# Optimization experiments

Measured on AMD Instinct MI355X. Metric: run time of the kernel, lower is better.

The kernel has to match this reference:

```python
import jax, jax.numpy as jnp
import numpy as np

N_NODES = 100000
N_EDGES = 1600000
IN_F = 16
C1, C2 = 32, 64
HID = 128
N_CLASSES = 10
NUM_LAYERS = 3


def setup_inputs() -> dict:
    key = jax.random.key(0)
    ks = jax.random.split(key, 20)
    s = 0.1
    inp = {
        "x": jax.random.normal(ks[0], (N_NODES, IN_F), dtype=jnp.float32),
        "edge_index": jax.random.randint(ks[1], (2, N_EDGES), 0, N_NODES, dtype=jnp.int64),
        "edge_attr": jax.random.uniform(ks[2], (N_EDGES, 1), dtype=jnp.float32),
        # conv1 (out=32): per-step weight [L, 32, 32], GRUCell params
        "W1": jax.random.normal(ks[3], (NUM_LAYERS, C1, C1), dtype=jnp.float32) * s,
        "Wih1": jax.random.normal(ks[4], (3 * C1, C1), dtype=jnp.float32) * s,
        "Whh1": jax.random.normal(ks[5], (3 * C1, C1), dtype=jnp.float32) * s,
        "bih1": jnp.zeros((3 * C1,), dtype=jnp.float32),
        "bhh1": jnp.zeros((3 * C1,), dtype=jnp.float32),
        # conv2 (out=64)
        "W2": jax.random.normal(ks[6], (NUM_LAYERS, C2, C2), dtype=jnp.float32) * s,
        "Wih2": jax.random.normal(ks[7], (3 * C2, C2), dtype=jnp.float32) * s,
        "Whh2": jax.random.normal(ks[8], (3 * C2, C2), dtype=jnp.float32) * s,
        "bih2": jnp.zeros((3 * C2,), dtype=jnp.float32),
        "bhh2": jnp.zeros((3 * C2,), dtype=jnp.float32),
        # MLP head
        "fc1_w": jax.random.normal(ks[9], (HID, C2), dtype=jnp.float32) * s,
        "fc1_b": jnp.zeros((HID,), dtype=jnp.float32),
        "fc2_w": jax.random.normal(ks[10], (N_CLASSES, HID), dtype=jnp.float32) * s,
        "fc2_b": jnp.zeros((N_CLASSES,), dtype=jnp.float32),
    }
    return inp


def _gru_cell(m, h, Wih, Whh, bih, bhh):
    gi = m @ Wih.T + bih
    gh = h @ Whh.T + bhh
    ir, iz, inn = jnp.split(gi, 3, axis=1)
    hr, hz, hn = jnp.split(gh, 3, axis=1)
    r = jax.nn.sigmoid(ir + hr)
    z = jax.nn.sigmoid(iz + hz)
    n = jnp.tanh(inn + r * hn)
    return (1.0 - z) * n + z * h


def _gated_graph_conv(x, edge_index, edge_weight, W, Wih, Whh, bih, bhh):
    # PyG GatedGraphConv with aggr='max'
    n, c = x.shape
    out_ch = W.shape[-1]
    h = jnp.pad(x, ((0, 0), (0, out_ch - c))) if c < out_ch else x
    src, dst = edge_index[0], edge_index[1]
    ew = edge_weight[:, None]
    for i in range(W.shape[0]):
        m = h @ W[i]
        msg = m[src] * ew                      # [E, out_ch] gather + scale
        agg = jax.ops.segment_max(msg, dst, num_segments=n)  # scatter-max
        agg = jnp.where(jnp.isfinite(agg), agg, 0.0)         # empty segs -> 0
        h = _gru_cell(agg, h, Wih, Whh, bih, bhh)
    return h


def reference(x, edge_index, edge_attr, W1, Wih1, Whh1, bih1, bhh1,
              W2, Wih2, Whh2, bih2, bhh2, fc1_w, fc1_b, fc2_w, fc2_b):
    ew = jnp.squeeze(edge_attr)
    h = jax.nn.elu(_gated_graph_conv(x, edge_index, ew, W1, Wih1, Whh1, bih1, bhh1))
    h = jax.nn.elu(_gated_graph_conv(h, edge_index, ew, W2, Wih2, Whh2, bih2, bhh2))
    h = jax.nn.elu(h @ fc1_w.T + fc1_b)
    logits = h @ fc2_w.T + fc2_b
    return jax.nn.log_softmax(logits, axis=1)
```

## Files before the change

kernel.cpp:

```cpp
#include <hip/hip_runtime.h>
#include <math.h>

#define N_NODES 100000
#define N_EDGES 1600000
#define SCAN_BS 1024
#define NBK 8
#define BKSH 14
#define NBINS (N_NODES*NBK)

typedef __attribute__((ext_vector_type(8))) short bf8_t;
typedef __attribute__((ext_vector_type(4))) float f4_t;
typedef unsigned short us;
typedef unsigned long long ull;

__device__ __forceinline__ float sigmoidf_(float x){ return 1.f/(1.f + expf(-x)); }
__device__ __forceinline__ float eluf_(float x){ return x > 0.f ? x : expm1f(x); }
__device__ __forceinline__ us f2bf(float x){
  unsigned u = __float_as_uint(x);
  unsigned r = u + 0x7FFFu + ((u>>16)&1u);
  return (us)(r>>16);
}
__device__ __forceinline__ float bf2f(us v){
  return __uint_as_float(((unsigned)v)<<16);
}

__global__ void prep_all(const float* __restrict__ Wih1, const float* __restrict__ Whh1,
                         const float* __restrict__ Wih2, const float* __restrict__ Whh2,
                         const float* __restrict__ W1,   const float* __restrict__ W2,
                         const float* __restrict__ fc1w, const float* __restrict__ fc2w,
                         const float* __restrict__ fc2b,
                         us* Wihb1, us* Whhb1, us* Wihb2, us* Whhb2,
                         us* Wtb1, us* Wtb2, us* fc1wb, us* fc2wpb, float* fc2bp){
  int i = blockIdx.x*256 + threadIdx.x;
  if (i < 3072) { Wihb1[i]=f2bf(Wih1[i]); return; } i -= 3072;
  if (i < 3072) { Whhb1[i]=f2bf(Whh1[i]); return; } i -= 3072;
  if (i < 12288){ Wihb2[i]=f2bf(Wih2[i]); return; } i -= 12288;
  if (i < 12288){ Whhb2[i]=f2bf(Whh2[i]); return; } i -= 12288;
  if (i < 3072) { int k=i%32, c=(i/32)%32, m=i/1024;
                  Wtb1[i]=f2bf(W1[m*1024 + k*32 + c]); return; } i -= 3072;
  if (i < 12288){ int k=i%64, c=(i/64)%64, m=i/4096;
                  Wtb2[i]=f2bf(W2[m*4096 + k*64 + c]); return; } i -= 12288;
  if (i < 8192) { fc1wb[i]=f2bf(fc1w[i]); return; } i -= 8192;
  if (i < 2048) { int c=i/128, k=i%128;
                  fc2wpb[i]=(c<10)?f2bf(fc2w[c*128+k]):(us)0; return; } i -= 2048;
  if (i < 16)   { fc2bp[i] = (i<10)? fc2b[i] : 0.f; }
}

__global__ void zero_counts(int* cnt, int* cur, int n){
  int i = blockIdx.x*blockDim.x + threadIdx.x;
  if (i < n){ cnt[i]=0; cur[i]=0; }
}
__global__ void count_kernel(const int* __restrict__ ei, int* __restrict__ cnt, int e){
  int i = blockIdx.x*blockDim.x + threadIdx.x;
  if (i < e){
    int s = ei[i], d = ei[N_EDGES + i];
    atomicAdd(&cnt[d*NBK + (s>>BKSH)], 1);
  }
}
__global__ void scan1_kernel(const int* __restrict__ cnt, int* __restrict__ pre,
                             int* __restrict__ bsum, int n){
  __shared__ int sh[SCAN_BS];
  int t = threadIdx.x, gi = blockIdx.x*SCAN_BS + t;
  int v = (gi < n) ? cnt[gi] : 0;
  sh[t] = v;
  __syncthreads();
  for (int off=1; off<SCAN_BS; off<<=1){
    int u = (t>=off)?sh[t-off]:0;
    __syncthreads();
    sh[t] += u;
    __syncthreads();
  }
  if (gi < n) pre[gi] = sh[t] - v;
  if (t == SCAN_BS-1) bsum[blockIdx.x] = sh[t];
}
__global__ void scan2_kernel(int* __restrict__ bsum, int nb){
  __shared__ int sh[1024];
  int t = threadIdx.x;
  int v = (t < nb) ? bsum[t] : 0;
  sh[t] = v;
  __syncthreads();
  for (int off=1; off<1024; off<<=1){
    int u = (t>=off)?sh[t-off]:0;
    __syncthreads();
    sh[t] += u;
    __syncthreads();
  }
  if (t < nb) bsum[t] = sh[t] - v;
}
__global__ void scan3_kernel(const int* __restrict__ pre, const int* __restrict__ bsum,
                             int* __restrict__ rs2, int total){
  int i = blockIdx.x*blockDim.x + threadIdx.x;
  if (i < total) rs2[i] = pre[i] + bsum[i/SCAN_BS];
  if (i == 0) rs2[total] = N_EDGES;
}
__global__ void scatter_kernel(const int* __restrict__ ei, const float* __restrict__ ea,
    const int* __restrict__ rs2, int* __restrict__ cur,
    long long* __restrict__ esrc, int e){
  int i0 = (blockIdx.x*blockDim.x + threadIdx.x)*2;
  #pragma unroll
  for (int j=0;j<2;j++){
    int i = i0 + j;
    if (i < e){
      int s = ei[i], d = ei[N_EDGES + i];
      int bin = d*NBK + (s>>BKSH);
      int p = rs2[bin] + atomicAdd(&cur[bin], 1);
      long long v = (long long)(unsigned)s
                  | ((long long)(unsigned)__float_as_int(ea[i]) << 32);
      __builtin_nontemporal_store(v, &esrc[p]);
    }
  }
}

__global__ void pad_x_kernel(const float* __restrict__ x, us* __restrict__ hb, int n){
  int i = blockIdx.x*blockDim.x + threadIdx.x;
  if (i < n*32){
    int node = i >> 5, c = i & 31;
    hb[i] = (c < 16) ? f2bf(x[node*16 + c]) : (us)0;
  }
}
__global__ void transition_kernel(const us* __restrict__ h1b, us* __restrict__ h2b, int n){
  int i = blockIdx.x*blockDim.x + threadIdx.x;
  if (i < n*64){
    int node = i >> 6, c = i & 63;
    h2b[i] = (c < 32) ? f2bf(eluf_(bf2f(h1b[node*32 + c]))) : (us)0;
  }
}

template<int C>
__global__ __launch_bounds__(256) void mgemm_mfma(const us* __restrict__ hb,
    const us* __restrict__ Wtb, us* __restrict__ mb, int n){
  constexpr int NT = C/16, KS = C/32;
  int l = threadIdx.x & 63, w = threadIdx.x >> 6;
  int mbase = blockIdx.x*64 + w*16;
  if (mbase >= n) return;
  int lr = l & 15, lk = (l >> 4)*8;
  f4_t acc[NT];
  #pragma unroll
  for (int t=0;t<NT;t++) acc[t] = f4_t{0.f,0.f,0.f,0.f};
  #pragma unroll
  for (int ks=0; ks<KS; ks++){
    int k0 = ks*32 + lk;
    bf8_t a = *(const bf8_t*)(hb + (size_t)(mbase+lr)*C + k0);
    #pragma unroll
    for (int t=0;t<NT;t++){
      bf8_t b = *(const bf8_t*)(Wtb + (size_t)(t*16+lr)*C + k0);
      acc[t] = __builtin_amdgcn_mfma_f32_16x16x32_bf16(a, b, acc[t], 0, 0, 0);
    }
  }
  int dr = (l>>4)*4;
  #pragma unroll
  for (int t=0;t<NT;t++){
    #pragma unroll
    for (int r=0;r<4;r++){
      int node = mbase + dr + r;
      if (node < n)
        mb[(size_t)node*C + t*16 + lr] = f2bf(acc[t][r]);
    }
  }
}

template<int C>
__global__ void agg_kernel(const us* __restrict__ mb, const int* __restrict__ rs2,
    const long long* __restrict__ esrc, us* __restrict__ aggb, int n_nodes){
  constexpr int GPN = C/8;
  int gid = blockIdx.x*blockDim.x + threadIdx.x;
  int nn = gid / GPN, g8 = gid % GPN;
  if (nn >= n_nodes) return;
  int s = rs2[nn*NBK], e = rs2[nn*NBK + NBK];
  float acc[8];
  #pragma unroll
  for (int j=0;j<8;j++) acc[j] = -__builtin_inff();
  const us* mbg = mb + g8*8;
  int i = s;
  for (; i+4<=e; i+=4){
    long long e0 = esrc[i], e1 = esrc[i+1], e2 = esrc[i+2], e3 = esrc[i+3];
    uint4 v0 = *(const uint4*)(mbg + (size_t)(unsigned)(e0 & 0xFFFFFFFF)*C);
    uint4 v1 = *(const uint4*)(mbg + (size_t)(unsigned)(e1 & 0xFFFFFFFF)*C);
    uint4 v2 = *(const uint4*)(mbg + (size_t)(unsigned)(e2 & 0xFFFFFFFF)*C);
    uint4 v3 = *(const uint4*)(mbg + (size_t)(unsigned)(e3 & 0xFFFFFFFF)*C);
    float w0 = __int_as_float((int)(e0>>32)), w1 = __int_as_float((int)(e1>>32));
    float w2 = __int_as_float((int)(e2>>32)), w3 = __int_as_float((int)(e3>>32));
    unsigned a0[4] = {v0.x, v0.y, v0.z, v0.w};
    unsigned a1[4] = {v1.x, v1.y, v1.z, v1.w};
    unsigned a2[4] = {v2.x, v2.y, v2.z, v2.w};
    unsigned a3[4] = {v3.x, v3.y, v3.z, v3.w};
    #pragma unroll
    for (int q=0;q<4;q++){
      float x0 = fmaxf(__uint_as_float(a0[q]<<16)*w0, __uint_as_float(a1[q]<<16)*w1);
      float x1 = fmaxf(__uint_as_float(a2[q]<<16)*w2, __uint_as_float(a3[q]<<16)*w3);
      float y0 = fmaxf(__uint_as_float(a0[q]&0xFFFF0000u)*w0, __uint_as_float(a1[q]&0xFFFF0000u)*w1);
      float y1 = fmaxf(__uint_as_float(a2[q]&0xFFFF0000u)*w2, __uint_as_float(a3[q]&0xFFFF0000u)*w3);
      acc[2*q]   = fmaxf(acc[2*q],   fmaxf(x0, x1));
      acc[2*q+1] = fmaxf(acc[2*q+1], fmaxf(y0, y1));
    }
  }
  for (; i<e; i++){
    long long e0 = esrc[i];
    uint4 v0 = *(const uint4*)(mbg + (size_t)(unsigned)(e0 & 0xFFFFFFFF)*C);
    float w0 = __int_as_float((int)(e0>>32));
    unsigned a0[4] = {v0.x, v0.y, v0.z, v0.w};
    #pragma unroll
    for (int q=0;q<4;q++){
      acc[2*q]   = fmaxf(acc[2*q],   __uint_as_float(a0[q]<<16)*w0);
      acc[2*q+1] = fmaxf(acc[2*q+1], __uint_as_float(a0[q]&0xFFFF0000u)*w0);
    }
  }
  unsigned r[8];
  #pragma unroll
  for (int j=0;j<8;j++) r[j] = (e > s) ? (unsigned)f2bf(acc[j]) : 0u;
  uint4 o;
  o.x = r[0] | (r[1]<<16); o.y = r[2] | (r[3]<<16);
  o.z = r[4] | (r[5]<<16); o.w = r[6] | (r[7]<<16);
  *(uint4*)(aggb + (size_t)nn*C + g8*8) = o;
}

template<int C, bool COMPUTE_M>
__global__ __launch_bounds__(256) void gru_mfma(
    const us* __restrict__ aggb, const us* __restrict__ hbin,
    const us* __restrict__ Wihb, const us* __restrict__ Whhb,
    const float* __restrict__ bih, const float* __restrict__ bhh,
    const us* __restrict__ Wtb_next,
    us* __restrict__ hbout, us* __restrict__ mbout, int n){
  constexpr int NT = 3*C/16;
  constexpr int KS = C/32;
  constexpr int CT = C/16;
  constexpr int TST = C + 8;
  constexpr int TSZ = COMPUTE_M ? 16*TST : 1;
  __shared__ us tlds[4][TSZ];
  int l = threadIdx.x & 63, w = threadIdx.x >> 6;
  int mbase = blockIdx.x*64 + w*16;
  int lr = l & 15, lk = (l >> 4)*8;
  f4_t accI[NT], accH[NT];
  #pragma unroll
  for (int t=0;t<NT;t++){ accI[t]=f4_t{0.f,0.f,0.f,0.f}; accH[t]=f4_t{0.f,0.f,0.f,0.f}; }
  #pragma unroll
  for (int ks=0; ks<KS; ks++){
    int k0 = ks*32 + lk;
    bf8_t aI = *(const bf8_t*)(aggb + (size_t)(mbase+lr)*C + k0);
    bf8_t aH = *(const bf8_t*)(hbin + (size_t)(mbase+lr)*C + k0);
    #pragma unroll
    for (int t=0;t<NT;t++){
      bf8_t bI = *(const bf8_t*)(Wihb + (size_t)(t*16+lr)*C + k0);
      accI[t] = __builtin_amdgcn_mfma_f32_16x16x32_bf16(aI, bI, accI[t], 0, 0, 0);
      bf8_t bH = *(const bf8_t*)(Whhb + (size_t)(t*16+lr)*C + k0);
      accH[t] = __builtin_amdgcn_mfma_f32_16x16x32_bf16(aH, bH, accH[t], 0, 0, 0);
    }
  }
  int dr = (l>>4)*4;
  us* tile = tlds[w];
  #pragma unroll
  for (int ct=0; ct<CT; ct++){
    int c = ct*16 + lr;
    float bR = bih[c],     cR = bhh[c];
    float bZ = bih[c+C],   cZ = bhh[c+C];
    float bN = bih[c+2*C], cN = bhh[c+2*C];
    #pragma unroll
    for (int r=0;r<4;r++){
      int i = mbase + dr + r;
      float giR = accI[ct][r] + bR,      ghR = accH[ct][r] + cR;
      float giZ = accI[CT+ct][r] + bZ,   ghZ = accH[CT+ct][r] + cZ;
      float giN = accI[2*CT+ct][r] + bN, ghN = accH[2*CT+ct][r] + cN;
      float rr = sigmoidf_(giR + ghR);
      float z  = sigmoidf_(giZ + ghZ);
      float nn = tanhf(giN + rr*ghN);
      float h  = bf2f(hbin[(size_t)i*C + c]);
      float ho = (1.f - z)*nn + z*h;
      us hob = f2bf(ho);
      if constexpr (COMPUTE_M)
        tile[(dr+r)*TST + c] = hob;
      if (i < n)
        hbout[(size_t)i*C + c] = hob;
    }
  }
  if constexpr (COMPUTE_M){
    __syncthreads();
    f4_t macc[CT];
    #pragma unroll
    for (int t=0;t<CT;t++) macc[t] = f4_t{0.f,0.f,0.f,0.f};
    #pragma unroll
    for (int ks=0; ks<KS; ks++){
      int k0 = ks*32 + lk;
      bf8_t a = *(const bf8_t*)(tile + lr*TST + k0);
      #pragma unroll
      for (int t=0;t<CT;t++){
        bf8_t b = *(const bf8_t*)(Wtb_next + (size_t)(t*16+lr)*C + k0);
        macc[t] = __builtin_amdgcn_mfma_f32_16x16x32_bf16(a, b, macc[t], 0, 0, 0);
      }
    }
    #pragma unroll
    for (int t=0;t<CT;t++){
      #pragma unroll
      for (int r=0;r<4;r++){
        int node = mbase + dr + r;
        if (node < n)
          mbout[(size_t)node*C + t*16 + lr] = f2bf(macc[t][r]);
      }
    }
  }
}

__global__ __launch_bounds__(256) void head_mfma(const us* __restrict__ h2b,
    const us* __restrict__ fc1wb, const float* __restrict__ fc1b,
    const us* __restrict__ fc2wpb, const float* __restrict__ fc2bp,
    float* __restrict__ out, int n){
  __shared__ __align__(16) us lds[4][16*136];
  int l = threadIdx.x & 63, w = threadIdx.x >> 6;
  int mbase = blockIdx.x*64 + w*16;
  int lr = l & 15, lk = (l >> 4)*8;
  int dr = (l>>4)*4;
  f4_t acc1[8];
  #pragma unroll
  for (int t=0;t<8;t++) acc1[t] = f4_t{0.f,0.f,0.f,0.f};
  #pragma unroll
  for (int ks=0; ks<2; ks++){
    int k0 = ks*32 + lk;
    bf8_t hv = *(const bf8_t*)(h2b + (size_t)(mbase+lr)*64 + k0);
    bf8_t a;
    #pragma unroll
    for (int j=0;j<8;j++)
      a[j] = (short)f2bf(eluf_(bf2f((us)hv[j])));
    #pragma unroll
    for (int t=0;t<8;t++){
      bf8_t b = *(const bf8_t*)(fc1wb + (size_t)(t*16+lr)*64 + k0);
      acc1[t] = __builtin_amdgcn_mfma_f32_16x16x32_bf16(a, b, acc1[t], 0, 0, 0);
    }
  }
  us* tile = lds[w];
  #pragma unroll
  for (int t=0;t<8;t++){
    float b1 = fc1b[t*16 + lr];
    #pragma unroll
    for (int r=0;r<4;r++)
      tile[(dr+r)*136 + t*16 + lr] = f2bf(eluf_(acc1[t][r] + b1));
  }
  __syncthreads();
  f4_t acc2 = f4_t{0.f,0.f,0.f,0.f};
  #pragma unroll
  for (int ks=0; ks<4; ks++){
    int k0 = ks*32 + lk;
    bf8_t a = *(const bf8_t*)(tile + lr*136 + k0);
    bf8_t b = *(const bf8_t*)(fc2wpb + (size_t)lr*128 + k0);
    acc2 = __builtin_amdgcn_mfma_f32_16x16x32_bf16(a, b, acc2, 0, 0, 0);
  }
  float b2 = fc2bp[lr];
  #pragma unroll
  for (int r=0;r<4;r++){
    float val = acc2[r] + b2;
    float vm = (lr < 10) ? val : -__builtin_inff();
    #pragma unroll
    for (int m=1;m<16;m<<=1) vm = fmaxf(vm, __shfl_xor(vm, m, 64));
    float ex = (lr < 10) ? expf(val - vm) : 0.f;
    #pragma unroll
    for (int m=1;m<16;m<<=1) ex += __shfl_xor(ex, m, 64);
    float lse = vm + logf(ex);
    int node = mbase + dr + r;
    if (lr < 10 && node < n) out[(size_t)node*10 + lr] = val - lse;
  }
}

extern "C" void kernel_launch(void* const* d_in, const int* in_sizes, int n_in,
                              void* d_out, int out_size, void* d_ws, size_t ws_size,
                              hipStream_t stream){
  const float* x    = (const float*)d_in[0];
  const int*   ei   = (const int*)  d_in[1];
  const float* ea   = (const float*)d_in[2];
  const float* W1   = (const float*)d_in[3];
  const float* Wih1 = (const float*)d_in[4];
  const float* Whh1 = (const float*)d_in[5];
  const float* bih1 = (const float*)d_in[6];
  const float* bhh1 = (const float*)d_in[7];
  const float* W2   = (const float*)d_in[8];
  const float* Wih2 = (const float*)d_in[9];
  const float* Whh2 = (const float*)d_in[10];
  const float* bih2 = (const float*)d_in[11];
  const float* bhh2 = (const float*)d_in[12];
  const float* fc1w = (const float*)d_in[13];
  const float* fc1b = (const float*)d_in[14];
  const float* fc2w = (const float*)d_in[15];
  const float* fc2b = (const float*)d_in[16];
  float* outp = (float*)d_out;

  char* ws = (char*)d_ws;
  size_t off = 0;
  auto alloc = [&](size_t bytes)->void*{
    void* p = ws + off;
    off += (bytes + 255) & ~size_t(255);
    return p;
  };
  us* hAb0    = (us*)alloc(sizeof(us)*N_NODES*32);
  us* hAb1    = (us*)alloc(sizeof(us)*N_NODES*32);
  us* hBb0    = (us*)alloc(sizeof(us)*N_NODES*64);
  us* hBb1    = (us*)alloc(sizeof(us)*N_NODES*64);
  us* mb      = (us*)alloc(sizeof(us)*N_NODES*64);
  us* aggb    = (us*)alloc(sizeof(us)*N_NODES*64);
  int* rs2    = (int*)alloc(sizeof(int)*(NBINS+1));
  int* cnt    = (int*)alloc(sizeof(int)*NBINS);
  int* cur    = (int*)alloc(sizeof(int)*NBINS);
  int* pre    = (int*)alloc(sizeof(int)*NBINS);
  int* bsum   = (int*)alloc(sizeof(int)*1024);
  long long* esrc = (long long*)alloc(sizeof(long long)*N_EDGES);
  us* Wihb1   = (us*)alloc(sizeof(us)*96*32);
  us* Whhb1   = (us*)alloc(sizeof(us)*96*32);
  us* Wihb2   = (us*)alloc(sizeof(us)*192*64);
  us* Whhb2   = (us*)alloc(sizeof(us)*192*64);
  us* Wtb1    = (us*)alloc(sizeof(us)*3*32*32);
  us* Wtb2    = (us*)alloc(sizeof(us)*3*64*64);
  us* fc1wb   = (us*)alloc(sizeof(us)*128*64);
  us* fc2wpb  = (us*)alloc(sizeof(us)*16*128);
  float* fc2bp= (float*)alloc(sizeof(float)*16);
  (void)ws_size; (void)in_sizes; (void)n_in; (void)out_size;

  const int n = N_NODES, e = N_EDGES;
  const int nbk = (NBINS + SCAN_BS - 1)/SCAN_BS;
  const int gblk = (n + 63)/64;

  prep_all<<<(56336+255)/256,256,0,stream>>>(Wih1, Whh1, Wih2, Whh2, W1, W2,
      fc1w, fc2w, fc2b, Wihb1, Whhb1, Wihb2, Whhb2, Wtb1, Wtb2, fc1wb, fc2wpb, fc2bp);

  zero_counts<<<(NBINS+255)/256,256,0,stream>>>(cnt, cur, NBINS);
  count_kernel<<<(e+255)/256,256,0,stream>>>(ei, cnt, e);
  scan1_kernel<<<nbk,SCAN_BS,0,stream>>>(cnt, pre, bsum, NBINS);
  scan2_kernel<<<1,1024,0,stream>>>(bsum, nbk);
  scan3_kernel<<<(NBINS+255)/256,256,0,stream>>>(pre, bsum, rs2, NBINS);
  scatter_kernel<<<(e/2+255)/256,256,0,stream>>>(ei, ea, rs2, cur, esrc, e);

  pad_x_kernel<<<(n*32+255)/256,256,0,stream>>>(x, hAb0, n);
  us* l1fin;
  {
    us* c0 = hAb0; us* c1 = hAb1;
    mgemm_mfma<32><<<gblk,256,0,stream>>>(c0, Wtb1, mb, n);
    for (int i=0;i<3;i++){
      agg_kernel<32><<<((long long)n*4+255)/256,256,0,stream>>>(mb, rs2, esrc, aggb, n);
      if (i < 2)
        gru_mfma<32,true><<<gblk,256,0,stream>>>(aggb, c0, Wihb1, Whhb1, bih1, bhh1,
                                                 Wtb1 + (i+1)*32*32, c1, mb, n);
      else
        gru_mfma<32,false><<<gblk,256,0,stream>>>(aggb, c0, Wihb1, Whhb1, bih1, bhh1,
                                                  nullptr, c1, nullptr, n);
      us* t = c0; c0 = c1; c1 = t;
    }
    l1fin = c0;
  }

  transition_kernel<<<(n*64+255)/256,256,0,stream>>>(l1fin, hBb0, n);

  us* l2fin;
  {
    us* c0 = hBb0; us* c1 = hBb1;
    mgemm_mfma<64><<<gblk,256,0,stream>>>(c0, Wtb2, mb, n);
    for (int i=0;i<3;i++){
      agg_kernel<64><<<((long long)n*8+255)/256,256,0,stream>>>(mb, rs2, esrc, aggb, n);
      if (i < 2)
        gru_mfma<64,true><<<gblk,256,0,stream>>>(aggb, c0, Wihb2, Whhb2, bih2, bhh2,
                                                 Wtb2 + (i+1)*64*64, c1, mb, n);
      else
        gru_mfma<64,false><<<gblk,256,0,stream>>>(aggb, c0, Wihb2, Whhb2, bih2, bhh2,
                                                  nullptr, c1, nullptr, n);
      us* t = c0; c0 = c1; c1 = t;
    }
    l2fin = c0;
  }

  head_mfma<<<gblk,256,0,stream>>>(l2fin, fc1wb, fc1b, fc2wpb, fc2bp, outp, n);
}
```

Before: 649.4 us.

## Fuse max-aggregation into GRU MFMA kernel and fold ELU transition into epilogue

The per-node gather/scale/max aggregation now runs inside the GRU kernel, writing directly into the MFMA A-fragment registers instead of going through a separate agg kernel and an aggb buffer. Double-buffered message arrays (mb0/mb1) remove the hazard between reading this step's messages and writing the next step's. The layer-1 to layer-2 ELU+pad transition moves into the last layer-1 GRU epilogue. This removes launches and aggregation-buffer round trips. In exchange, each gather pass uses only 64 threads per 16 nodes with low per-thread parallelism, so latency hiding and occupancy may suffer, and in-wave degree imbalance can stall warps.

```diff
diff --git a/kernel.cpp b/kernel.cpp
--- a/kernel.cpp
+++ b/kernel.cpp
@@ -118,13 +118,6 @@
     hb[i] = (c < 16) ? f2bf(x[node*16 + c]) : (us)0;
   }
 }
-__global__ void transition_kernel(const us* __restrict__ h1b, us* __restrict__ h2b, int n){
-  int i = blockIdx.x*blockDim.x + threadIdx.x;
-  if (i < n*64){
-    int node = i >> 6, c = i & 63;
-    h2b[i] = (c < 32) ? f2bf(eluf_(bf2f(h1b[node*32 + c]))) : (us)0;
-  }
-}
 
 template<int C>
 __global__ __launch_bounds__(256) void mgemm_mfma(const us* __restrict__ hb,
@@ -159,64 +152,10 @@
   }
 }
 
-template<int C>
-__global__ void agg_kernel(const us* __restrict__ mb, const int* __restrict__ rs2,
-    const long long* __restrict__ esrc, us* __restrict__ aggb, int n_nodes){
-  constexpr int GPN = C/8;
-  int gid = blockIdx.x*blockDim.x + threadIdx.x;
-  int nn = gid / GPN, g8 = gid % GPN;
-  if (nn >= n_nodes) return;
-  int s = rs2[nn*NBK], e = rs2[nn*NBK + NBK];
-  float acc[8];
-  #pragma unroll
-  for (int j=0;j<8;j++) acc[j] = -__builtin_inff();
-  const us* mbg = mb + g8*8;
-  int i = s;
-  for (; i+4<=e; i+=4){
-    long long e0 = esrc[i], e1 = esrc[i+1], e2 = esrc[i+2], e3 = esrc[i+3];
-    uint4 v0 = *(const uint4*)(mbg + (size_t)(unsigned)(e0 & 0xFFFFFFFF)*C);
-    uint4 v1 = *(const uint4*)(mbg + (size_t)(unsigned)(e1 & 0xFFFFFFFF)*C);
-    uint4 v2 = *(const uint4*)(mbg + (size_t)(unsigned)(e2 & 0xFFFFFFFF)*C);
-    uint4 v3 = *(const uint4*)(mbg + (size_t)(unsigned)(e3 & 0xFFFFFFFF)*C);
-    float w0 = __int_as_float((int)(e0>>32)), w1 = __int_as_float((int)(e1>>32));
-    float w2 = __int_as_float((int)(e2>>32)), w3 = __int_as_float((int)(e3>>32));
-    unsigned a0[4] = {v0.x, v0.y, v0.z, v0.w};
-    unsigned a1[4] = {v1.x, v1.y, v1.z, v1.w};
-    unsigned a2[4] = {v2.x, v2.y, v2.z, v2.w};
-    unsigned a3[4] = {v3.x, v3.y, v3.z, v3.w};
-    #pragma unroll
-    for (int q=0;q<4;q++){
-      float x0 = fmaxf(__uint_as_float(a0[q]<<16)*w0, __uint_as_float(a1[q]<<16)*w1);
-      float x1 = fmaxf(__uint_as_float(a2[q]<<16)*w2, __uint_as_float(a3[q]<<16)*w3);
-      float y0 = fmaxf(__uint_as_float(a0[q]&0xFFFF0000u)*w0, __uint_as_float(a1[q]&0xFFFF0000u)*w1);
-      float y1 = fmaxf(__uint_as_float(a2[q]&0xFFFF0000u)*w2, __uint_as_float(a3[q]&0xFFFF0000u)*w3);
-      acc[2*q]   = fmaxf(acc[2*q],   fmaxf(x0, x1));
-      acc[2*q+1] = fmaxf(acc[2*q+1], fmaxf(y0, y1));
-    }
-  }
-  for (; i<e; i++){
-    long long e0 = esrc[i];
-    uint4 v0 = *(const uint4*)(mbg + (size_t)(unsigned)(e0 & 0xFFFFFFFF)*C);
-    float w0 = __int_as_float((int)(e0>>32));
-    unsigned a0[4] = {v0.x, v0.y, v0.z, v0.w};
-    #pragma unroll
-    for (int q=0;q<4;q++){
-      acc[2*q]   = fmaxf(acc[2*q],   __uint_as_float(a0[q]<<16)*w0);
-      acc[2*q+1] = fmaxf(acc[2*q+1], __uint_as_float(a0[q]&0xFFFF0000u)*w0);
-    }
-  }
-  unsigned r[8];
-  #pragma unroll
-  for (int j=0;j<8;j++) r[j] = (e > s) ? (unsigned)f2bf(acc[j]) : 0u;
-  uint4 o;
-  o.x = r[0] | (r[1]<<16); o.y = r[2] | (r[3]<<16);
-  o.z = r[4] | (r[5]<<16); o.w = r[6] | (r[7]<<16);
-  *(uint4*)(aggb + (size_t)nn*C + g8*8) = o;
-}
-
-template<int C, bool COMPUTE_M>
-__global__ __launch_bounds__(256) void gru_mfma(
-    const us* __restrict__ aggb, const us* __restrict__ hbin,
+template<int C, bool COMPUTE_M, bool TRANS>
+__global__ __launch_bounds__(256) void gru_fused(
+    const us* __restrict__ mbin, const us* __restrict__ hbin,
+    const int* __restrict__ rs2, const long long* __restrict__ esrc,
     const us* __restrict__ Wihb, const us* __restrict__ Whhb,
     const float* __restrict__ bih, const float* __restrict__ bhh,
     const us* __restrict__ Wtb_next,
@@ -224,24 +163,79 @@
   constexpr int NT = 3*C/16;
   constexpr int KS = C/32;
   constexpr int CT = C/16;
+  constexpr int NCH = 8*KS;
   constexpr int TST = C + 8;
   constexpr int TSZ = COMPUTE_M ? 16*TST : 1;
   __shared__ us tlds[4][TSZ];
   int l = threadIdx.x & 63, w = threadIdx.x >> 6;
   int mbase = blockIdx.x*64 + w*16;
   int lr = l & 15, lk = (l >> 4)*8;
+
+  int node = mbase + lr;
+  bool valid = node < n;
+  int s = 0, e = 0;
+  if (valid){ s = rs2[node*NBK]; e = rs2[node*NBK + NBK]; }
+  float ga[NCH];
+  #pragma unroll
+  for (int j=0;j<NCH;j++) ga[j] = -__builtin_inff();
+  {
+    const us* m0 = mbin + lk;
+    int i = s;
+    for (; i+2<=e; i+=2){
+      long long e0 = esrc[i], e1 = esrc[i+1];
+      size_t r0 = (size_t)(unsigned)(e0 & 0xFFFFFFFF)*C;
+      size_t r1 = (size_t)(unsigned)(e1 & 0xFFFFFFFF)*C;
+      float w0 = __int_as_float((int)(e0>>32)), w1 = __int_as_float((int)(e1>>32));
+      #pragma unroll
+      for (int ks=0; ks<KS; ks++){
+        uint4 v0 = *(const uint4*)(m0 + r0 + ks*32);
+        uint4 v1 = *(const uint4*)(m0 + r1 + ks*32);
+        unsigned a0[4] = {v0.x, v0.y, v0.z, v0.w};
+        unsigned a1[4] = {v1.x, v1.y, v1.z, v1.w};
+        #pragma unroll
+        for (int q=0;q<4;q++){
+          float x0 = fmaxf(__uint_as_float(a0[q]<<16)*w0, __uint_as_float(a1[q]<<16)*w1);
+          float y0 = fmaxf(__uint_as_float(a0[q]&0xFFFF0000u)*w0, __uint_as_float(a1[q]&0xFFFF0000u)*w1);
+          ga[ks*8+2*q]   = fmaxf(ga[ks*8+2*q],   x0);
+          ga[ks*8+2*q+1] = fmaxf(ga[ks*8+2*q+1], y0);
+        }
+      }
+    }
+    if (i < e){
+      long long e0 = esrc[i];
+      size_t r0 = (size_t)(unsigned)(e0 & 0xFFFFFFFF)*C;
+      float w0 = __int_as_float((int)(e0>>32));
+      #pragma unroll
+      for (int ks=0; ks<KS; ks++){
+        uint4 v0 = *(const uint4*)(m0 + r0 + ks*32);
+        unsigned a0[4] = {v0.x, v0.y, v0.z, v0.w};
+        #pragma unroll
+        for (int q=0;q<4;q++){
+          ga[ks*8+2*q]   = fmaxf(ga[ks*8+2*q],   __uint_as_float(a0[q]<<16)*w0);
+          ga[ks*8+2*q+1] = fmaxf(ga[ks*8+2*q+1], __uint_as_float(a0[q]&0xFFFF0000u)*w0);
+        }
+      }
+    }
+  }
+  bf8_t aggfrag[KS];
+  #pragma unroll
+  for (int ks=0; ks<KS; ks++){
+    #pragma unroll
+    for (int j=0;j<8;j++)
+      aggfrag[ks][j] = (short)((e > s) ? f2bf(ga[ks*8+j]) : (us)0);
+  }
+
   f4_t accI[NT], accH[NT];
   #pragma unroll
   for (int t=0;t<NT;t++){ accI[t]=f4_t{0.f,0.f,0.f,0.f}; accH[t]=f4_t{0.f,0.f,0.f,0.f}; }
   #pragma unroll
   for (int ks=0; ks<KS; ks++){
     int k0 = ks*32 + lk;
-    bf8_t aI = *(const bf8_t*)(aggb + (size_t)(mbase+lr)*C + k0);
     bf8_t aH = *(const bf8_t*)(hbin + (size_t)(mbase+lr)*C + k0);
     #pragma unroll
     for (int t=0;t<NT;t++){
       bf8_t bI = *(const bf8_t*)(Wihb + (size_t)(t*16+lr)*C + k0);
-      accI[t] = __builtin_amdgcn_mfma_f32_16x16x32_bf16(aI, bI, accI[t], 0, 0, 0);
+      accI[t] = __builtin_amdgcn_mfma_f32_16x16x32_bf16(aggfrag[ks], bI, accI[t], 0, 0, 0);
       bf8_t bH = *(const bf8_t*)(Whhb + (size_t)(t*16+lr)*C + k0);
       accH[t] = __builtin_amdgcn_mfma_f32_16x16x32_bf16(aH, bH, accH[t], 0, 0, 0);
     }
@@ -268,8 +262,14 @@
       us hob = f2bf(ho);
       if constexpr (COMPUTE_M)
         tile[(dr+r)*TST + c] = hob;
-      if (i < n)
-        hbout[(size_t)i*C + c] = hob;
+      if (i < n){
+        if constexpr (TRANS){
+          hbout[(size_t)i*64 + c] = f2bf(eluf_(ho));
+          hbout[(size_t)i*64 + 32 + c] = 0;
+        } else {
+          hbout[(size_t)i*C + c] = hob;
+        }
+      }
     }
   }
   if constexpr (COMPUTE_M){
@@ -291,9 +291,9 @@
     for (int t=0;t<CT;t++){
       #pragma unroll
       for (int r=0;r<4;r++){
-        int node = mbase + dr + r;
-        if (node < n)
-          mbout[(size_t)node*C + t*16 + lr] = f2bf(macc[t][r]);
+        int nd = mbase + dr + r;
+        if (nd < n)
+          mbout[(size_t)nd*C + t*16 + lr] = f2bf(macc[t][r]);
       }
     }
   }
@@ -391,8 +391,8 @@
   us* hAb1    = (us*)alloc(sizeof(us)*N_NODES*32);
   us* hBb0    = (us*)alloc(sizeof(us)*N_NODES*64);
   us* hBb1    = (us*)alloc(sizeof(us)*N_NODES*64);
-  us* mb      = (us*)alloc(sizeof(us)*N_NODES*64);
-  us* aggb    = (us*)alloc(sizeof(us)*N_NODES*64);
+  us* mb0     = (us*)alloc(sizeof(us)*N_NODES*64);
+  us* mb1     = (us*)alloc(sizeof(us)*N_NODES*64);
   int* rs2    = (int*)alloc(sizeof(int)*(NBINS+1));
   int* cnt    = (int*)alloc(sizeof(int)*NBINS);
   int* cur    = (int*)alloc(sizeof(int)*NBINS);
@@ -425,41 +425,21 @@
   scatter_kernel<<<(e/2+255)/256,256,0,stream>>>(ei, ea, rs2, cur, esrc, e);
 
   pad_x_kernel<<<(n*32+255)/256,256,0,stream>>>(x, hAb0, n);
-  us* l1fin;
-  {
-    us* c0 = hAb0; us* c1 = hAb1;
-    mgemm_mfma<32><<<gblk,256,0,stream>>>(c0, Wtb1, mb, n);
-    for (int i=0;i<3;i++){
-      agg_kernel<32><<<((long long)n*4+255)/256,256,0,stream>>>(mb, rs2, esrc, aggb, n);
-      if (i < 2)
-        gru_mfma<32,true><<<gblk,256,0,stream>>>(aggb, c0, Wihb1, Whhb1, bih1, bhh1,
-                                                 Wtb1 + (i+1)*32*32, c1, mb, n);
-      else
-        gru_mfma<32,false><<<gblk,256,0,stream>>>(aggb, c0, Wihb1, Whhb1, bih1, bhh1,
-                                                  nullptr, c1, nullptr, n);
-      us* t = c0; c0 = c1; c1 = t;
-    }
-    l1fin = c0;
-  }
-
-  transition_kernel<<<(n*64+255)/256,256,0,stream>>>(l1fin, hBb0, n);
-
-  us* l2fin;
-  {
-    us* c0 = hBb0; us* c1 = hBb1;
-    mgemm_mfma<64><<<gblk,256,0,stream>>>(c0, Wtb2, mb, n);
-    for (int i=0;i<3;i++){
-      agg_kernel<64><<<((long long)n*8+255)/256,256,0,stream>>>(mb, rs2, esrc, aggb, n);
-      if (i < 2)
-        gru_mfma<64,true><<<gblk,256,0,stream>>>(aggb, c0, Wihb2, Whhb2, bih2, bhh2,
-                                                 Wtb2 + (i+1)*64*64, c1, mb, n);
-      else
-        gru_mfma<64,false><<<gblk,256,0,stream>>>(aggb, c0, Wihb2, Whhb2, bih2, bhh2,
-                                                  nullptr, c1, nullptr, n);
-      us* t = c0; c0 = c1; c1 = t;
-    }
-    l2fin = c0;
-  }
-
-  head_mfma<<<gblk,256,0,stream>>>(l2fin, fc1wb, fc1b, fc2wpb, fc2bp, outp, n);
-}
+  mgemm_mfma<32><<<gblk,256,0,stream>>>(hAb0, Wtb1, mb0, n);
+  gru_fused<32,true,false><<<gblk,256,0,stream>>>(mb0, hAb0, rs2, esrc,
+      Wihb1, Whhb1, bih1, bhh1, Wtb1 + 1*32*32, hAb1, mb1, n);
+  gru_fused<32,true,false><<<gblk,256,0,stream>>>(mb1, hAb1, rs2, esrc,
+      Wihb1, Whhb1, bih1, bhh1, Wtb1 + 2*32*32, hAb0, mb0, n);
+  gru_fused<32,false,true><<<gblk,256,0,stream>>>(mb0, hAb0, rs2, esrc,
+      Wihb1, Whhb1, bih1, bhh1, nullptr, hBb0, nullptr, n);
+
+  mgemm_mfma<64><<<gblk,256,0,stream>>>(hBb0, Wtb2, mb0, n);
+  gru_fused<64,true,false><<<gblk,256,0,stream>>>(mb0, hBb0, rs2, esrc,
+      Wihb2, Whhb2, bih2, bhh2, Wtb2 + 1*64*64, hBb1, mb1, n);
+  gru_fused<64,true,false><<<gblk,256,0,stream>>>(mb1, hBb1, rs2, esrc,
+      Wihb2, Whhb2, bih2, bhh2, Wtb2 + 2*64*64, hBb0, mb0, n);
+  gru_fused<64,false,false><<<gblk,256,0,stream>>>(mb0, hBb0, rs2, esrc,
+      Wihb2, Whhb2, bih2, bhh2, nullptr, hBb1, nullptr, n);
+
+  head_mfma<<<gblk,256,0,stream>>>(hBb1, fc1wb, fc1b, fc2wpb, fc2bp, outp, n);
+}
```

After: 710.4 us (median of 3 runs). 1.09x slower.
